# Performance work log

Measured on AMD Instinct MI355X. Metric: run time of the kernel, lower is better.

The kernel has to match this reference:

```python
import jax, jax.numpy as jnp
import numpy as np

N = 50000
E = 625000
D_IN, D_HID, D_OUT = 128, 128, 64


def setup_inputs() -> dict:
    key = jax.random.key(0)
    k1, k2, k3, k4 = jax.random.split(key, 4)
    x = jax.random.normal(k1, (N, D_IN), dtype=jnp.float32)
    edge_index = jax.random.randint(k2, (2, E), 0, N, dtype=jnp.int32)
    # Glorot-ish init for linear weights (PyG lin has no bias; bias added after agg)
    W1 = jax.random.normal(k3, (D_HID, D_IN), dtype=jnp.float32) / np.sqrt(D_IN)
    b1 = jnp.zeros((D_HID,), dtype=jnp.float32)
    W2 = jax.random.normal(k4, (D_OUT, D_HID), dtype=jnp.float32) / np.sqrt(D_HID)
    b2 = jnp.zeros((D_OUT,), dtype=jnp.float32)
    return {"x": x, "edge_index": edge_index, "W1": W1, "b1": b1, "W2": W2, "b2": b2}


def _gcn_conv(x, W, b, src, dst, n):
    # GCNConv: h = x @ W^T; out[dst] += norm * h[src]; out += b
    # src/dst already include self-loops; symmetric normalization deg^{-1/2}.
    ones = jnp.ones(src.shape[0], dtype=x.dtype)
    deg = jax.ops.segment_sum(ones, dst, num_segments=n)
    dinv = jnp.where(deg > 0, jax.lax.rsqrt(deg), 0.0)
    norm = dinv[src] * dinv[dst]                      # [E+N]
    h = x @ W.T                                        # [N, d_out]
    msg = norm[:, None] * h[src]                       # [E+N, d_out]
    out = jax.ops.segment_sum(msg, dst, num_segments=n)
    return out + b


def reference(x, edge_index, W1, b1, W2, b2):
    n = x.shape[0]
    loops = jnp.arange(n, dtype=edge_index.dtype)
    src = jnp.concatenate([edge_index[0], loops])      # add self-loops
    dst = jnp.concatenate([edge_index[1], loops])
    h = _gcn_conv(x, W1, b1, src, dst, n)
    h = jax.nn.relu(h)
    out = _gcn_conv(h, W2, b2, src, dst, n)
    return out
```

## Files before the change

kernel.cpp:

```cpp
#include <hip/hip_runtime.h>
#include <hip/hip_bf16.h>


typedef __attribute__((ext_vector_type(8))) __bf16 bf16x8;
typedef __attribute__((ext_vector_type(8))) unsigned short ushort8;
typedef __attribute__((ext_vector_type(4))) float floatx4;

static __device__ __forceinline__ float bf2f(unsigned short s) {
    unsigned u = ((unsigned)s) << 16;
    return __builtin_bit_cast(float, u);
}
static __device__ __forceinline__ unsigned short f2bf(float f) {
    unsigned u = __builtin_bit_cast(unsigned, f);
    unsigned r = (u + 0x7FFFu + ((u >> 16) & 1u)) >> 16;
    return (unsigned short)r;
}
static __device__ __forceinline__ void ld8f(const void* p, size_t idx, int isbf, float* o) {
    if (isbf) {
        ushort8 t = __builtin_bit_cast(ushort8, *(const int4*)((const unsigned short*)p + idx));
        #pragma unroll
        for (int j = 0; j < 8; ++j) o[j] = bf2f(t[j]);
    } else {
        const float* f = (const float*)p + idx;
        float4 a = *(const float4*)f;
        float4 b = *(const float4*)(f + 4);
        o[0]=a.x; o[1]=a.y; o[2]=a.z; o[3]=a.w; o[4]=b.x; o[5]=b.y; o[6]=b.z; o[7]=b.w;
    }
}
static __device__ __forceinline__ int4 ld8frag(const void* p, size_t idx, int isbf) {
    if (isbf) {
        return *(const int4*)((const unsigned short*)p + idx);
    } else {
        const float* f = (const float*)p + idx;
        float4 a = *(const float4*)f;
        float4 b = *(const float4*)(f + 4);
        ushort8 t;
        t[0]=f2bf(a.x); t[1]=f2bf(a.y); t[2]=f2bf(a.z); t[3]=f2bf(a.w);
        t[4]=f2bf(b.x); t[5]=f2bf(b.y); t[6]=f2bf(b.z); t[7]=f2bf(b.w);
        return __builtin_bit_cast(int4, t);
    }
}
static __device__ __forceinline__ float bread(const void* p, int i, int isbf) {
    return isbf ? bf2f(((const unsigned short*)p)[i]) : ((const float*)p)[i];
}

__global__ void k_detect(const unsigned* __restrict__ xw, int* flag) {
    __shared__ int red[256];
    int t = threadIdx.x;
    int cnt = 0;
    #pragma unroll
    for (int i = 0; i < 16; ++i) {
        unsigned w = xw[t * 16 + i];
        unsigned exp = (w >> 7) & 0xFFu;
        cnt += (exp <= 0x84u) ? 1 : 0;
    }
    red[t] = cnt;
    __syncthreads();
    for (int s = 128; s > 0; s >>= 1) {
        if (t < s) red[t] += red[t + s];
        __syncthreads();
    }
    if (t == 0) flag[0] = (red[0] >= 3686) ? 1 : 0;
}

__global__ void k_zero(int* cnt, int n) {
    int i = blockIdx.x * 256 + threadIdx.x;
    if (i < n) cnt[i] = 0;
}
__global__ void k_count(const int* __restrict__ dst, int* __restrict__ cnt, int E) {
    int e = blockIdx.x * 256 + threadIdx.x;
    if (e < E) atomicAdd(&cnt[dst[e]], 1);
}

__global__ __launch_bounds__(256) void k_scanA(
    const int* __restrict__ cnt, int* __restrict__ partial, int N)
{
    int b = blockIdx.x, t = threadIdx.x;
    int base = b * 1024 + t * 4;
    int s = 0;
    if (base + 3 < N) {
        int4 v = *(const int4*)&cnt[base];
        s = v.x + v.y + v.z + v.w;
    } else {
        for (int j = 0; j < 4; ++j) { int i = base + j; if (i < N) s += cnt[i]; }
    }
    #pragma unroll
    for (int d = 1; d < 64; d <<= 1) s += __shfl_down(s, d, 64);
    __shared__ int ws[4];
    int lane = t & 63, wid = t >> 6;
    if (lane == 0) ws[wid] = s;
    __syncthreads();
    if (t == 0) partial[b] = ws[0] + ws[1] + ws[2] + ws[3];
}
__global__ void k_scanB(const int* __restrict__ partial, int* __restrict__ prefix, int nb) {
    int lane = threadIdx.x;
    int carry = 0;
    int nch = (nb + 63) / 64;
    for (int c = 0; c < nch; ++c) {
        int i = c * 64 + lane;
        int v = (i < nb) ? partial[i] : 0;
        int x = v;
        #pragma unroll
        for (int d = 1; d < 64; d <<= 1) {
            int u = __shfl_up(x, d, 64);
            if (lane >= d) x += u;
        }
        if (i < nb) prefix[i] = carry + x - v;
        carry += __shfl(x, 63, 64);
    }
    if (lane == 0) prefix[nb] = carry;
}
__global__ __launch_bounds__(256) void k_scanC(
    const int* __restrict__ cnt, const int* __restrict__ prefix,
    int* __restrict__ off, int* __restrict__ cursor, float* __restrict__ dinv,
    int N, int nb)
{
    int b = blockIdx.x, t = threadIdx.x, lane = t & 63, wid = t >> 6;
    int base = b * 1024 + t * 4;
    int v[4], s = 0;
    #pragma unroll
    for (int j = 0; j < 4; ++j) {
        int i = base + j;
        v[j] = (i < N) ? cnt[i] : 0;
        s += v[j];
    }
    int x = s;
    #pragma unroll
    for (int d = 1; d < 64; d <<= 1) {
        int u = __shfl_up(x, d, 64);
        if (lane >= d) x += u;
    }
    __shared__ int wtot[4], woff[4];
    if (lane == 63) wtot[wid] = x;
    __syncthreads();
    if (t == 0) {
        int a = 0;
        #pragma unroll
        for (int w = 0; w < 4; ++w) { woff[w] = a; a += wtot[w]; }
    }
    __syncthreads();
    int excl = prefix[b] + woff[wid] + (x - s);
    #pragma unroll
    for (int j = 0; j < 4; ++j) {
        int i = base + j;
        if (i < N) {
            off[i] = excl;
            cursor[i] = excl;
            dinv[i] = rsqrtf(1.0f + (float)v[j]);
            excl += v[j];
        }
    }
    if (b == 0 && t == 0) off[N] = prefix[nb];
}

__global__ void k_scatter(const int* __restrict__ src, const int* __restrict__ dst,
                          int* __restrict__ cursor, int* __restrict__ bucket, int E) {
    int e = blockIdx.x * 256 + threadIdx.x;
    if (e >= E) return;
    int pos = atomicAdd(&cursor[dst[e]], 1);
    bucket[pos] = src[e];
}

__global__ __launch_bounds__(256) void k_gather1(
    const void* __restrict__ x, const float* __restrict__ dinv,
    const int* __restrict__ off, const int* __restrict__ bucket,
    float* __restrict__ buf, int N, const int* __restrict__ flag)
{
    int isbf = *flag;
    int gid = blockIdx.x * 256 + threadIdx.x;
    int node = gid >> 4, p = gid & 15;
    if (node >= N) return;
    float di = dinv[node];
    float acc[8], va[8], vb[8];
    ld8f(x, (size_t)node * 128 + p * 8, isbf, va);
    float w0 = di * di;
    #pragma unroll
    for (int j = 0; j < 8; ++j) acc[j] = w0 * va[j];
    int it = off[node], s1 = off[node + 1];
    for (; it + 1 < s1; it += 2) {
        int sa = bucket[it], sb = bucket[it + 1];
        float wa = di * dinv[sa], wb = di * dinv[sb];
        ld8f(x, (size_t)sa * 128 + p * 8, isbf, va);
        ld8f(x, (size_t)sb * 128 + p * 8, isbf, vb);
        #pragma unroll
        for (int j = 0; j < 8; ++j) acc[j] += wa * va[j] + wb * vb[j];
    }
    if (it < s1) {
        int sa = bucket[it];
        float wa = di * dinv[sa];
        ld8f(x, (size_t)sa * 128 + p * 8, isbf, va);
        #pragma unroll
        for (int j = 0; j < 8; ++j) acc[j] += wa * va[j];
    }
    float* o = &buf[(size_t)node * 128 + p * 8];
    float4 a = {acc[0], acc[1], acc[2], acc[3]};
    float4 b = {acc[4], acc[5], acc[6], acc[7]};
    *(float4*)o = a;
    *(float4*)(o + 4) = b;
}

__global__ __launch_bounds__(256) void k_gemm1(
    float* buf, const void* __restrict__ W1, const void* __restrict__ b1,
    int N, const int* __restrict__ flag)
{
    int isbf = *flag;
    __shared__ int4 lds[2048];
    int tid = threadIdx.x;
    for (int u = tid; u < 2048; u += 256) {
        int nt = u >> 8, kt = (u >> 6) & 3, lane = u & 63;
        int so = (nt * 16 + (lane & 15)) * 128 + kt * 32 + ((lane >> 4) << 3);
        lds[u] = ld8frag(W1, so, isbf);
    }
    __syncthreads();

    int wave = tid >> 6, lane = tid & 63;
    int ntile = (N + 15) >> 4;
    int tile = blockIdx.x * 4 + wave;
    if (tile >= ntile) return;
    int m = lane & 15, quad = lane >> 4;

    int arow = tile * 16 + m;
    if (arow >= N) arow = N - 1;
    bf16x8 a[4];
    for (int kt = 0; kt < 4; ++kt) {
        const float* p = &buf[(size_t)arow * 128 + kt * 32 + quad * 8];
        float4 f0 = *(const float4*)p;
        float4 f1 = *(const float4*)(p + 4);
        ushort8 t;
        t[0]=f2bf(f0.x); t[1]=f2bf(f0.y); t[2]=f2bf(f0.z); t[3]=f2bf(f0.w);
        t[4]=f2bf(f1.x); t[5]=f2bf(f1.y); t[6]=f2bf(f1.z); t[7]=f2bf(f1.w);
        a[kt] = __builtin_bit_cast(bf16x8, t);
    }

    floatx4 acc[8];
    floatx4 z = {0.f, 0.f, 0.f, 0.f};
    for (int nt = 0; nt < 8; ++nt) acc[nt] = z;
    for (int kt = 0; kt < 4; ++kt)
        for (int nt = 0; nt < 8; ++nt) {
            bf16x8 b = __builtin_bit_cast(bf16x8, lds[nt * 256 + kt * 64 + lane]);
            acc[nt] = __builtin_amdgcn_mfma_f32_16x16x32_bf16(a[kt], b, acc[nt], 0, 0, 0);
        }

    unsigned short* h1 = (unsigned short*)buf;
    int rbase = tile * 16 + quad * 4;
    for (int nt = 0; nt < 8; ++nt) {
        int col = nt * 16 + m;
        float bb = bread(b1, col, isbf);
        for (int r = 0; r < 4; ++r) {
            int orow = rbase + r;
            if (orow < N) {
                float v = acc[nt][r] + bb;
                h1[(size_t)orow * 256 + col] = f2bf(fmaxf(v, 0.f));
            }
        }
    }
}

__global__ __launch_bounds__(256) void k_gemm2(
    float* buf, const void* __restrict__ W2, int N, const int* __restrict__ flag)
{
    int isbf = *flag;
    __shared__ int4 lds[1024];
    int tid = threadIdx.x;
    for (int u = tid; u < 1024; u += 256) {
        int nt = u >> 8, kt = (u >> 6) & 3, lane = u & 63;
        int so = (nt * 16 + (lane & 15)) * 128 + kt * 32 + ((lane >> 4) << 3);
        lds[u] = ld8frag(W2, so, isbf);
    }
    __syncthreads();

    int wave = tid >> 6, lane = tid & 63;
    int ntile = (N + 15) >> 4;
    int tile = blockIdx.x * 4 + wave;
    if (tile >= ntile) return;
    int m = lane & 15, quad = lane >> 4;

    const unsigned short* h1 = (const unsigned short*)buf;
    int arow = tile * 16 + m;
    if (arow >= N) arow = N - 1;
    bf16x8 a[4];
    for (int kt = 0; kt < 4; ++kt)
        a[kt] = __builtin_bit_cast(bf16x8, *(const int4*)&h1[(size_t)arow * 256 + kt * 32 + quad * 8]);

    floatx4 acc[4];
    floatx4 z = {0.f, 0.f, 0.f, 0.f};
    for (int nt = 0; nt < 4; ++nt) acc[nt] = z;
    for (int kt = 0; kt < 4; ++kt)
        for (int nt = 0; nt < 4; ++nt) {
            bf16x8 b = __builtin_bit_cast(bf16x8, lds[nt * 256 + kt * 64 + lane]);
            acc[nt] = __builtin_amdgcn_mfma_f32_16x16x32_bf16(a[kt], b, acc[nt], 0, 0, 0);
        }

    unsigned short* h2 = (unsigned short*)buf;
    int rbase = tile * 16 + quad * 4;
    for (int nt = 0; nt < 4; ++nt) {
        int col = nt * 16 + m;
        for (int r = 0; r < 4; ++r) {
            int orow = rbase + r;
            if (orow < N)
                h2[(size_t)orow * 256 + col] = f2bf(acc[nt][r]);
        }
    }
}

__global__ __launch_bounds__(256) void k_gather2(
    const float* __restrict__ buf, const float* __restrict__ dinv,
    const int* __restrict__ off, const int* __restrict__ bucket,
    const void* __restrict__ b2, void* __restrict__ out, int N,
    const int* __restrict__ flag)
{
    int isbf = *flag;
    int gid = blockIdx.x * 256 + threadIdx.x;
    int node = gid >> 3, p = gid & 7;
    if (node >= N) return;
    const unsigned short* h2 = (const unsigned short*)buf;
    float di = dinv[node];
    float acc[8];
    {
        ushort8 t = __builtin_bit_cast(ushort8, *(const int4*)&h2[(size_t)node * 256 + p * 8]);
        float w0 = di * di;
        #pragma unroll
        for (int j = 0; j < 8; ++j) acc[j] = w0 * bf2f(t[j]);
    }
    int it = off[node], s1 = off[node + 1];
    for (; it + 1 < s1; it += 2) {
        int sa = bucket[it], sb = bucket[it + 1];
        float wa = di * dinv[sa], wb = di * dinv[sb];
        ushort8 ta = __builtin_bit_cast(ushort8, *(const int4*)&h2[(size_t)sa * 256 + p * 8]);
        ushort8 tb = __builtin_bit_cast(ushort8, *(const int4*)&h2[(size_t)sb * 256 + p * 8]);
        #pragma unroll
        for (int j = 0; j < 8; ++j) acc[j] += wa * bf2f(ta[j]) + wb * bf2f(tb[j]);
    }
    if (it < s1) {
        int sa = bucket[it];
        float wa = di * dinv[sa];
        ushort8 ta = __builtin_bit_cast(ushort8, *(const int4*)&h2[(size_t)sa * 256 + p * 8]);
        #pragma unroll
        for (int j = 0; j < 8; ++j) acc[j] += wa * bf2f(ta[j]);
    }
    #pragma unroll
    for (int j = 0; j < 8; ++j) acc[j] += bread(b2, p * 8 + j, isbf);
    if (isbf) {
        ushort8 o;
        #pragma unroll
        for (int j = 0; j < 8; ++j) o[j] = f2bf(acc[j]);
        *(int4*)((unsigned short*)out + (size_t)node * 64 + p * 8) = __builtin_bit_cast(int4, o);
    } else {
        float* fo = (float*)out + (size_t)node * 64 + p * 8;
        float4 a = {acc[0], acc[1], acc[2], acc[3]};
        float4 b = {acc[4], acc[5], acc[6], acc[7]};
        *(float4*)fo = a;
        *(float4*)(fo + 4) = b;
    }
}

extern "C" void kernel_launch(void* const* d_in, const int* in_sizes, int n_in,
                              void* d_out, int out_size, void* d_ws, size_t ws_size,
                              hipStream_t stream) {
    const void* x  = d_in[0];
    const int*  ei = (const int*)d_in[1];
    const void* W1 = d_in[2];
    const void* b1 = d_in[3];
    const void* W2 = d_in[4];
    const void* b2 = d_in[5];

    int N = in_sizes[0] / 128;
    int E = in_sizes[1] / 2;
    const int* srcI = ei;
    const int* dstI = ei + E;

    int nb = (N + 1023) / 1024;

    char* base = (char*)d_ws;
    size_t o = 0;
    auto take = [&](size_t bytes) { size_t r = o; o += (bytes + 255) & ~(size_t)255; return r; };
    int*   flag    = (int*)  (base + take(4));
    int*   cnt     = (int*)  (base + take((size_t)N * 4));
    int*   off     = (int*)  (base + take((size_t)(N + 1) * 4));
    int*   cursor  = (int*)  (base + take((size_t)N * 4));
    float* dinv    = (float*)(base + take((size_t)N * 4));
    int*   partial = (int*)  (base + take((size_t)nb * 4));
    int*   prefix  = (int*)  (base + take((size_t)(nb + 1) * 4));
    int*   bucket  = (int*)  (base + take((size_t)E * 4));
    float* buf     = (float*)(base + take((size_t)N * 512));

    int ntile = (N + 15) / 16;
    int gemmBlocks = (ntile + 3) / 4;

    k_detect<<<1, 256, 0, stream>>>((const unsigned*)x, flag);
    k_zero<<<(N + 255) / 256, 256, 0, stream>>>(cnt, N);
    k_count<<<(E + 255) / 256, 256, 0, stream>>>(dstI, cnt, E);
    k_scanA<<<nb, 256, 0, stream>>>(cnt, partial, N);
    k_scanB<<<1, 64, 0, stream>>>(partial, prefix, nb);
    k_scanC<<<nb, 256, 0, stream>>>(cnt, prefix, off, cursor, dinv, N, nb);
    k_scatter<<<(E + 255) / 256, 256, 0, stream>>>(srcI, dstI, cursor, bucket, E);
    k_gather1<<<(N * 16 + 255) / 256, 256, 0, stream>>>(x, dinv, off, bucket, buf, N, flag);
    k_gemm1<<<gemmBlocks, 256, 0, stream>>>(buf, W1, b1, N, flag);
    k_gemm2<<<gemmBlocks, 256, 0, stream>>>(buf, W2, N, flag);
    k_gather2<<<(N * 8 + 255) / 256, 256, 0, stream>>>(buf, dinv, off, bucket, b2, d_out, N, flag);
}
```

Before: 246.6 us.

## Fuse GEMM1 and GEMM2 via LDS tile, merge count/detect and drop scanB

Fuses the two dense GEMMs into one kernel. The ReLU'd hidden tile stays in per-wave LDS and the W2 fragments are held in registers, so the hidden activations never round-trip through global memory. It also merges the dtype-detect kernel into the edge-count kernel and replaces the zero kernel with a memset. The separate scanB kernel goes away: each scanC block serially sums the block partials itself. This cuts launch count and global traffic, at the cost of higher register/LDS use in the fused GEMM and a redundant serial prefix loop per block.

```diff
diff --git a/kernel.cpp b/kernel.cpp
--- a/kernel.cpp
+++ b/kernel.cpp
@@ -44,31 +44,31 @@
     return isbf ? bf2f(((const unsigned short*)p)[i]) : ((const float*)p)[i];
 }
 
-__global__ void k_detect(const unsigned* __restrict__ xw, int* flag) {
-    __shared__ int red[256];
-    int t = threadIdx.x;
-    int cnt = 0;
-    #pragma unroll
-    for (int i = 0; i < 16; ++i) {
-        unsigned w = xw[t * 16 + i];
-        unsigned exp = (w >> 7) & 0xFFu;
-        cnt += (exp <= 0x84u) ? 1 : 0;
-    }
-    red[t] = cnt;
-    __syncthreads();
-    for (int s = 128; s > 0; s >>= 1) {
-        if (t < s) red[t] += red[t + s];
+__global__ __launch_bounds__(256) void k_countdet(
+    const int* __restrict__ dst, int* __restrict__ cnt, int E, int EB,
+    const unsigned* __restrict__ xw, int* __restrict__ flag)
+{
+    int b = blockIdx.x;
+    if (b == EB) {
+        __shared__ int red[256];
+        int t = threadIdx.x;
+        int c = 0;
+        #pragma unroll
+        for (int i = 0; i < 16; ++i) {
+            unsigned w = xw[t * 16 + i];
+            unsigned exp = (w >> 7) & 0xFFu;
+            c += (exp <= 0x84u) ? 1 : 0;
+        }
+        red[t] = c;
         __syncthreads();
-    }
-    if (t == 0) flag[0] = (red[0] >= 3686) ? 1 : 0;
-}
-
-__global__ void k_zero(int* cnt, int n) {
-    int i = blockIdx.x * 256 + threadIdx.x;
-    if (i < n) cnt[i] = 0;
-}
-__global__ void k_count(const int* __restrict__ dst, int* __restrict__ cnt, int E) {
-    int e = blockIdx.x * 256 + threadIdx.x;
+        for (int s = 128; s > 0; s >>= 1) {
+            if (t < s) red[t] += red[t + s];
+            __syncthreads();
+        }
+        if (t == 0) flag[0] = (red[0] >= 3686) ? 1 : 0;
+        return;
+    }
+    int e = b * 256 + threadIdx.x;
     if (e < E) atomicAdd(&cnt[dst[e]], 1);
 }
 
@@ -92,30 +92,19 @@
     __syncthreads();
     if (t == 0) partial[b] = ws[0] + ws[1] + ws[2] + ws[3];
 }
-__global__ void k_scanB(const int* __restrict__ partial, int* __restrict__ prefix, int nb) {
-    int lane = threadIdx.x;
-    int carry = 0;
-    int nch = (nb + 63) / 64;
-    for (int c = 0; c < nch; ++c) {
-        int i = c * 64 + lane;
-        int v = (i < nb) ? partial[i] : 0;
-        int x = v;
-        #pragma unroll
-        for (int d = 1; d < 64; d <<= 1) {
-            int u = __shfl_up(x, d, 64);
-            if (lane >= d) x += u;
-        }
-        if (i < nb) prefix[i] = carry + x - v;
-        carry += __shfl(x, 63, 64);
-    }
-    if (lane == 0) prefix[nb] = carry;
-}
+
 __global__ __launch_bounds__(256) void k_scanC(
-    const int* __restrict__ cnt, const int* __restrict__ prefix,
+    const int* __restrict__ cnt, const int* __restrict__ partial,
     int* __restrict__ off, int* __restrict__ cursor, float* __restrict__ dinv,
     int N, int nb)
 {
+    __shared__ int s_pref, s_tot;
     int b = blockIdx.x, t = threadIdx.x, lane = t & 63, wid = t >> 6;
+    if (t == 0) {
+        int s = 0, pb = 0;
+        for (int i = 0; i < nb; ++i) { if (i == b) pb = s; s += partial[i]; }
+        s_pref = pb; s_tot = s;
+    }
     int base = b * 1024 + t * 4;
     int v[4], s = 0;
     #pragma unroll
@@ -139,7 +128,7 @@
         for (int w = 0; w < 4; ++w) { woff[w] = a; a += wtot[w]; }
     }
     __syncthreads();
-    int excl = prefix[b] + woff[wid] + (x - s);
+    int excl = s_pref + woff[wid] + (x - s);
     #pragma unroll
     for (int j = 0; j < 4; ++j) {
         int i = base + j;
@@ -150,7 +139,7 @@
             excl += v[j];
         }
     }
-    if (b == 0 && t == 0) off[N] = prefix[nb];
+    if (b == 0 && t == 0) off[N] = s_tot;
 }
 
 __global__ void k_scatter(const int* __restrict__ src, const int* __restrict__ dst,
@@ -199,29 +188,37 @@
     *(float4*)(o + 4) = b;
 }
 
-__global__ __launch_bounds__(256) void k_gemm1(
+__global__ __launch_bounds__(256) void k_gemm12(
     float* buf, const void* __restrict__ W1, const void* __restrict__ b1,
-    int N, const int* __restrict__ flag)
+    const void* __restrict__ W2, int N, const int* __restrict__ flag)
 {
     int isbf = *flag;
-    __shared__ int4 lds[2048];
+    __shared__ int4 w1f[2048];
+    __shared__ unsigned short h1t[4][16 * 136];
     int tid = threadIdx.x;
     for (int u = tid; u < 2048; u += 256) {
         int nt = u >> 8, kt = (u >> 6) & 3, lane = u & 63;
         int so = (nt * 16 + (lane & 15)) * 128 + kt * 32 + ((lane >> 4) << 3);
-        lds[u] = ld8frag(W1, so, isbf);
-    }
-    __syncthreads();
-
-    int wave = tid >> 6, lane = tid & 63;
+        w1f[u] = ld8frag(W1, so, isbf);
+    }
+    int wave = tid >> 6, lane = tid & 63, m = lane & 15, quad = lane >> 4;
+
+    int4 w2r[4][4];
+    #pragma unroll
+    for (int nt = 0; nt < 4; ++nt)
+        #pragma unroll
+        for (int kt = 0; kt < 4; ++kt)
+            w2r[nt][kt] = ld8frag(W2, (nt * 16 + m) * 128 + kt * 32 + quad * 8, isbf);
+    __syncthreads();
+
     int ntile = (N + 15) >> 4;
     int tile = blockIdx.x * 4 + wave;
-    if (tile >= ntile) return;
-    int m = lane & 15, quad = lane >> 4;
-
-    int arow = tile * 16 + m;
+    int tcl = (tile < ntile) ? tile : (ntile - 1);
+    int arow = tcl * 16 + m;
     if (arow >= N) arow = N - 1;
+
     bf16x8 a[4];
+    #pragma unroll
     for (int kt = 0; kt < 4; ++kt) {
         const float* p = &buf[(size_t)arow * 128 + kt * 32 + quad * 8];
         float4 f0 = *(const float4*)p;
@@ -231,74 +228,55 @@
         t[4]=f2bf(f1.x); t[5]=f2bf(f1.y); t[6]=f2bf(f1.z); t[7]=f2bf(f1.w);
         a[kt] = __builtin_bit_cast(bf16x8, t);
     }
-
     floatx4 acc[8];
     floatx4 z = {0.f, 0.f, 0.f, 0.f};
+    #pragma unroll
     for (int nt = 0; nt < 8; ++nt) acc[nt] = z;
+    #pragma unroll
     for (int kt = 0; kt < 4; ++kt)
+        #pragma unroll
         for (int nt = 0; nt < 8; ++nt) {
-            bf16x8 b = __builtin_bit_cast(bf16x8, lds[nt * 256 + kt * 64 + lane]);
+            bf16x8 b = __builtin_bit_cast(bf16x8, w1f[nt * 256 + kt * 64 + lane]);
             acc[nt] = __builtin_amdgcn_mfma_f32_16x16x32_bf16(a[kt], b, acc[nt], 0, 0, 0);
         }
-
-    unsigned short* h1 = (unsigned short*)buf;
-    int rbase = tile * 16 + quad * 4;
+    #pragma unroll
     for (int nt = 0; nt < 8; ++nt) {
         int col = nt * 16 + m;
         float bb = bread(b1, col, isbf);
+        #pragma unroll
         for (int r = 0; r < 4; ++r) {
-            int orow = rbase + r;
-            if (orow < N) {
-                float v = acc[nt][r] + bb;
-                h1[(size_t)orow * 256 + col] = f2bf(fmaxf(v, 0.f));
+            float v = acc[nt][r] + bb;
+            h1t[wave][(quad * 4 + r) * 136 + col] = f2bf(fmaxf(v, 0.f));
+        }
+    }
+    __syncthreads();
+
+    bf16x8 a2[4];
+    #pragma unroll
+    for (int kt = 0; kt < 4; ++kt)
+        a2[kt] = __builtin_bit_cast(bf16x8, *(const int4*)&h1t[wave][m * 136 + kt * 32 + quad * 8]);
+    floatx4 acc2[4];
+    #pragma unroll
+    for (int nt = 0; nt < 4; ++nt) acc2[nt] = z;
+    #pragma unroll
+    for (int kt = 0; kt < 4; ++kt)
+        #pragma unroll
+        for (int nt = 0; nt < 4; ++nt) {
+            bf16x8 b = __builtin_bit_cast(bf16x8, w2r[nt][kt]);
+            acc2[nt] = __builtin_amdgcn_mfma_f32_16x16x32_bf16(a2[kt], b, acc2[nt], 0, 0, 0);
+        }
+    if (tile < ntile) {
+        unsigned short* h2 = (unsigned short*)buf;
+        int rbase = tcl * 16 + quad * 4;
+        #pragma unroll
+        for (int nt = 0; nt < 4; ++nt) {
+            int col = nt * 16 + m;
+            #pragma unroll
+            for (int r = 0; r < 4; ++r) {
+                int orow = rbase + r;
+                if (orow < N)
+                    h2[(size_t)orow * 256 + col] = f2bf(acc2[nt][r]);
             }
-        }
-    }
-}
-
-__global__ __launch_bounds__(256) void k_gemm2(
-    float* buf, const void* __restrict__ W2, int N, const int* __restrict__ flag)
-{
-    int isbf = *flag;
-    __shared__ int4 lds[1024];
-    int tid = threadIdx.x;
-    for (int u = tid; u < 1024; u += 256) {
-        int nt = u >> 8, kt = (u >> 6) & 3, lane = u & 63;
-        int so = (nt * 16 + (lane & 15)) * 128 + kt * 32 + ((lane >> 4) << 3);
-        lds[u] = ld8frag(W2, so, isbf);
-    }
-    __syncthreads();
-
-    int wave = tid >> 6, lane = tid & 63;
-    int ntile = (N + 15) >> 4;
-    int tile = blockIdx.x * 4 + wave;
-    if (tile >= ntile) return;
-    int m = lane & 15, quad = lane >> 4;
-
-    const unsigned short* h1 = (const unsigned short*)buf;
-    int arow = tile * 16 + m;
-    if (arow >= N) arow = N - 1;
-    bf16x8 a[4];
-    for (int kt = 0; kt < 4; ++kt)
-        a[kt] = __builtin_bit_cast(bf16x8, *(const int4*)&h1[(size_t)arow * 256 + kt * 32 + quad * 8]);
-
-    floatx4 acc[4];
-    floatx4 z = {0.f, 0.f, 0.f, 0.f};
-    for (int nt = 0; nt < 4; ++nt) acc[nt] = z;
-    for (int kt = 0; kt < 4; ++kt)
-        for (int nt = 0; nt < 4; ++nt) {
-            bf16x8 b = __builtin_bit_cast(bf16x8, lds[nt * 256 + kt * 64 + lane]);
-            acc[nt] = __builtin_amdgcn_mfma_f32_16x16x32_bf16(a[kt], b, acc[nt], 0, 0, 0);
-        }
-
-    unsigned short* h2 = (unsigned short*)buf;
-    int rbase = tile * 16 + quad * 4;
-    for (int nt = 0; nt < 4; ++nt) {
-        int col = nt * 16 + m;
-        for (int r = 0; r < 4; ++r) {
-            int orow = rbase + r;
-            if (orow < N)
-                h2[(size_t)orow * 256 + col] = f2bf(acc[nt][r]);
         }
     }
 }
@@ -370,6 +348,7 @@
     const int* dstI = ei + E;
 
     int nb = (N + 1023) / 1024;
+    int EB = (E + 255) / 256;
 
     char* base = (char*)d_ws;
     size_t o = 0;
@@ -380,22 +359,18 @@
     int*   cursor  = (int*)  (base + take((size_t)N * 4));
     float* dinv    = (float*)(base + take((size_t)N * 4));
     int*   partial = (int*)  (base + take((size_t)nb * 4));
-    int*   prefix  = (int*)  (base + take((size_t)(nb + 1) * 4));
     int*   bucket  = (int*)  (base + take((size_t)E * 4));
     float* buf     = (float*)(base + take((size_t)N * 512));
 
     int ntile = (N + 15) / 16;
     int gemmBlocks = (ntile + 3) / 4;
 
-    k_detect<<<1, 256, 0, stream>>>((const unsigned*)x, flag);
-    k_zero<<<(N + 255) / 256, 256, 0, stream>>>(cnt, N);
-    k_count<<<(E + 255) / 256, 256, 0, stream>>>(dstI, cnt, E);
+    hipMemsetAsync(cnt, 0, (size_t)N * 4, stream);
+    k_countdet<<<EB + 1, 256, 0, stream>>>(dstI, cnt, E, EB, (const unsigned*)x, flag);
     k_scanA<<<nb, 256, 0, stream>>>(cnt, partial, N);
-    k_scanB<<<1, 64, 0, stream>>>(partial, prefix, nb);
-    k_scanC<<<nb, 256, 0, stream>>>(cnt, prefix, off, cursor, dinv, N, nb);
-    k_scatter<<<(E + 255) / 256, 256, 0, stream>>>(srcI, dstI, cursor, bucket, E);
+    k_scanC<<<nb, 256, 0, stream>>>(cnt, partial, off, cursor, dinv, N, nb);
+    k_scatter<<<EB, 256, 0, stream>>>(srcI, dstI, cursor, bucket, E);
     k_gather1<<<(N * 16 + 255) / 256, 256, 0, stream>>>(x, dinv, off, bucket, buf, N, flag);
-    k_gemm1<<<gemmBlocks, 256, 0, stream>>>(buf, W1, b1, N, flag);
-    k_gemm2<<<gemmBlocks, 256, 0, stream>>>(buf, W2, N, flag);
+    k_gemm12<<<gemmBlocks, 256, 0, stream>>>(buf, W1, b1, W2, N, flag);
     k_gather2<<<(N * 8 + 255) / 256, 256, 0, stream>>>(buf, dinv, off, bucket, b2, d_out, N, flag);
 }
```

Result: no change. 246.8 us (+0.1%).
